# Kernel optimization log

Measured on AMD Instinct MI355X. Metric: run time of the kernel, lower is better.

Reference implementation:

```python
import jax, jax.numpy as jnp
import numpy as np

B_, L_, H_, N_ = 8, 1024, 1024, 64

def setup_inputs() -> dict:
    key = jax.random.key(0)
    k1, k2, k3, k4 = jax.random.split(key, 4)
    return {
        "samples": jax.random.normal(k1, (B_, L_, 3 * H_), dtype=jnp.float32),
        "label_one_hot": jax.random.uniform(k2, (B_, L_, N_), dtype=jnp.float32),
        "predict": jax.random.normal(k3, (B_, L_, N_), dtype=jnp.float32),
        "W": jax.random.normal(k4, (H_, 3 * H_), dtype=jnp.float32) * (1.0 / np.sqrt(3 * H_)),
        "b_proj": jnp.zeros((H_,), dtype=jnp.float32),
    }

def reference(samples, label_one_hot, predict, W, b_proj):
    # projection: Linear(3H -> H)
    s = jnp.einsum("blk,hk->blh", samples, W) + b_proj          # [b,L,H]
    # dense similarity graph with diagonal masked out, row-softmax
    graph = jnp.einsum("blh,bmh->blm", s, s)                     # [b,L,L]
    L = graph.shape[1]
    eye = jnp.eye(L, dtype=graph.dtype)
    A = jax.nn.softmax(graph - 1e5 * eye, axis=-1)               # [b,L,L]
    # centered masked labels
    sup = label_one_hot
    row_has = (jnp.sum(sup, axis=-1) > 0.5).astype(sup.dtype)    # [b,L]
    total = jnp.sum(row_has, axis=-1)[:, None]                   # [b,1]
    avg = (jnp.sum(sup, axis=-2) / total)[:, None, :]            # [b,1,N]
    B0 = (sup - avg) * row_has[..., None]                        # [b,L,N]
    # diagonal inverse-degree scaling (elementwise, no dense diag matmul)
    d = 1.0 / (jnp.sum(A, axis=-1) + 1e-10)                      # [b,L]
    P = d[:, :, None] * jnp.swapaxes(A, -1, -2)                  # [b,L,L]
    Db = d[:, :, None] * B0                                      # [b,L,N]
    # 6-step power-iteration scan with residual injection at t==3
    ut = jnp.zeros_like(B0)
    for t in range(1, 7):
        ut = jnp.einsum("blm,bmn->bln", P, ut) + Db
        if t == 3:
            ut = ut + predict  # dropout is identity in eval mode
    return ut

if __name__ == "__main__":
    out = reference(**setup_inputs())
    print(out.shape, out.dtype)
```

## Files before the change

### kernel.cpp

```cpp
#include <hip/hip_runtime.h>


typedef _Float16 f16_t;
typedef f16_t f16x4 __attribute__((ext_vector_type(4)));
typedef f16_t f16x8 __attribute__((ext_vector_type(8)));
typedef float floatx4 __attribute__((ext_vector_type(4)));

__device__ __forceinline__ void async_copy16(const void* g, void* l) {
  __builtin_amdgcn_global_load_lds(
      (const __attribute__((address_space(1))) void*)g,
      (__attribute__((address_space(3))) void*)l, 16, 0, 0);
}

__device__ __forceinline__ f16_t hi_of(float x) { return (f16_t)x; }
__device__ __forceinline__ f16_t lo_of(float x, f16_t h) {
  return (f16_t)(x - (float)h);
}

__global__ __launch_bounds__(256) void prep_kernel(
    const float* __restrict__ W, f16_t* __restrict__ Whi, f16_t* __restrict__ Wlo,
    const float* __restrict__ samples, f16_t* __restrict__ SampH)
{
  const int bx = blockIdx.x, tid = threadIdx.x;
  if (bx < 3072) {
    const int i = bx * 256 + tid;
    float4 v = ((const float4*)W)[i];
    v.x *= 32.f; v.y *= 32.f; v.z *= 32.f; v.w *= 32.f;
    f16x4 h, l;
    f16_t h0 = hi_of(v.x); h[0] = h0; l[0] = lo_of(v.x, h0);
    f16_t h1 = hi_of(v.y); h[1] = h1; l[1] = lo_of(v.y, h1);
    f16_t h2 = hi_of(v.z); h[2] = h2; l[2] = lo_of(v.z, h2);
    f16_t h3 = hi_of(v.w); h[3] = h3; l[3] = lo_of(v.w, h3);
    *(f16x4*)(Whi + (size_t)i * 4) = h;
    *(f16x4*)(Wlo + (size_t)i * 4) = l;
  } else {
    const int i = (bx - 3072) * 256 + tid;
    const float4 v = ((const float4*)samples)[i];
    f16x4 h;
    h[0] = (f16_t)v.x; h[1] = (f16_t)v.y; h[2] = (f16_t)v.z; h[3] = (f16_t)v.w;
    *(f16x4*)(SampH + (size_t)i * 4) = h;
  }
}

template <int CMODE>
__global__ __launch_bounds__(256) void gemm_mfma(
    const f16_t* __restrict__ AhiG,
    const f16_t* __restrict__ BhiG, const f16_t* __restrict__ BloG,
    const float* __restrict__ bias,
    float* __restrict__ Cf, f16_t* __restrict__ Chi, f16_t* __restrict__ Clo,
    int M, int N, int K, long long sA, long long sB, long long sC, float cscale)
{
  AhiG += (long long)blockIdx.z * sA;
  BhiG += (long long)blockIdx.z * sB;
  BloG += (long long)blockIdx.z * sB;
  if (CMODE == 1) Cf += (long long)blockIdx.z * sC;

  __shared__ __align__(16) char smem[49152];
  f16_t* AsHi = (f16_t*)smem;
  f16_t* BsHi = (f16_t*)(smem + 16384);
  f16_t* BsLo = (f16_t*)(smem + 32768);

  const int tid = threadIdx.x;
  const int lane = tid & 63;
  const int wave = tid >> 6;
  const int wm = wave >> 1, wn = wave & 1;

  int m0, n0;
  if (CMODE == 0) {
    m0 = blockIdx.y * 128;
    n0 = blockIdx.x * 128;
  } else {
    int idx = blockIdx.x, i = 0, accu = 0;
    while (accu + i + 1 <= idx) { accu += i + 1; ++i; }
    m0 = i * 128;
    n0 = (idx - accu) * 128;
  }

  const int fr = lane & 15;
  const int kg = (lane >> 4) * 8;
  const int aoff = (wm * 64 + fr) * 32 + kg;
  const int boff = (wn * 64 + fr) * 32 + kg;

  floatx4 acc[4][4] = {};

  for (int k0 = 0; k0 < K; k0 += 64) {
    __syncthreads();
#pragma unroll
    for (int it = 0; it < 4; ++it) {
      const int cb = it * 256 + wave * 64;
      const int c = cb + lane;
      const int kk = c >> 9;
      const int row = (c >> 2) & 127;
      const int kc = kk * 32 + (c & 3) * 8;
      const size_t ga = (size_t)(m0 + row) * K + k0 + kc;
      const size_t gb = (size_t)(n0 + row) * K + k0 + kc;
      async_copy16(AhiG + ga, (char*)AsHi + (size_t)cb * 16);
      async_copy16(BhiG + gb, (char*)BsHi + (size_t)cb * 16);
      async_copy16(BloG + gb, (char*)BsLo + (size_t)cb * 16);
    }
    __syncthreads();

#pragma unroll
    for (int kk = 0; kk < 2; ++kk) {
      f16x8 ah[4], bh[4], bl[4];
#pragma unroll
      for (int t = 0; t < 4; ++t) {
        ah[t] = *(const f16x8*)&AsHi[kk * 4096 + aoff + t * 512];
        bh[t] = *(const f16x8*)&BsHi[kk * 4096 + boff + t * 512];
        bl[t] = *(const f16x8*)&BsLo[kk * 4096 + boff + t * 512];
      }
#pragma unroll
      for (int i = 0; i < 4; ++i)
#pragma unroll
        for (int j = 0; j < 4; ++j) {
          acc[i][j] = __builtin_amdgcn_mfma_f32_16x16x32_f16(ah[i], bh[j], acc[i][j], 0, 0, 0);
          acc[i][j] = __builtin_amdgcn_mfma_f32_16x16x32_f16(ah[i], bl[j], acc[i][j], 0, 0, 0);
        }
    }
  }

  const int mr = (lane >> 4) * 4;
#pragma unroll
  for (int j = 0; j < 4; ++j) {
    const int n = n0 + wn * 64 + j * 16 + fr;
    const float bj = (CMODE == 0) ? bias[n] : 0.f;
#pragma unroll
    for (int i = 0; i < 4; ++i) {
#pragma unroll
      for (int r = 0; r < 4; ++r) {
        const int m = m0 + wm * 64 + i * 16 + mr + r;
        float v = acc[i][j][r];
        if (CMODE == 0) {
          v = v * cscale + bj;
          f16_t h = hi_of(v);
          Chi[(size_t)m * N + n] = h;
          Clo[(size_t)m * N + n] = lo_of(v, h);
        } else {
          if (m == n) v -= 1e5f;
          Cf[(size_t)m * N + n] = v;
        }
      }
    }
  }

  if (CMODE == 1 && m0 != n0) {
    float* T = (float*)smem;
#pragma unroll
    for (int mc = 0; mc < 4; ++mc) {
      __syncthreads();
      if (wm == (mc >> 1)) {
        const int ibase = (mc & 1) * 2;
#pragma unroll
        for (int di = 0; di < 2; ++di) {
#pragma unroll
          for (int j = 0; j < 4; ++j) {
            const int nl = wn * 64 + j * 16 + fr;
#pragma unroll
            for (int r = 0; r < 4; ++r) {
              const int mloc = di * 16 + mr + r;
              T[nl * 36 + mloc] = acc[ibase + di][j][r];
            }
          }
        }
      }
      __syncthreads();
      const int row = tid >> 1, half = tid & 1;
      const float* src = &T[row * 36 + half * 16];
      float* dst = Cf + (size_t)(n0 + row) * N + m0 + mc * 32 + half * 16;
#pragma unroll
      for (int q = 0; q < 16; ++q) dst[q] = src[q];
    }
  }
}

__global__ __launch_bounds__(256) void rowstats_kernel(
    const float* __restrict__ G, float* __restrict__ mx, float* __restrict__ inv)
{
  __shared__ float red[4];
  const int tid = threadIdx.x;
  const float* g = G + (size_t)blockIdx.x * 1024;
  const float4 v = ((const float4*)g)[tid];

  float m = fmaxf(fmaxf(v.x, v.y), fmaxf(v.z, v.w));
#pragma unroll
  for (int off = 32; off > 0; off >>= 1) m = fmaxf(m, __shfl_down(m, off));
  if ((tid & 63) == 0) red[tid >> 6] = m;
  __syncthreads();
  m = fmaxf(fmaxf(red[0], red[1]), fmaxf(red[2], red[3]));
  __syncthreads();

  float s = __expf(v.x - m) + __expf(v.y - m) + __expf(v.z - m) + __expf(v.w - m);
#pragma unroll
  for (int off = 32; off > 0; off >>= 1) s += __shfl_down(s, off);
  if ((tid & 63) == 0) red[tid >> 6] = s;
  __syncthreads();
  if (tid == 0) {
    mx[blockIdx.x] = m;
    inv[blockIdx.x] = 1.0f / (red[0] + red[1] + red[2] + red[3]);
  }
}

__global__ __launch_bounds__(256) void make_at_kernel(
    const float* __restrict__ G, const float* __restrict__ mx,
    const float* __restrict__ inv, f16_t* __restrict__ At)
{
  const int row = blockIdx.x;
  const int b = row >> 10;
  const int tid = threadIdx.x;
  const float4 g = ((const float4*)(G + (size_t)row * 1024))[tid];
  const float4 m = ((const float4*)(mx + b * 1024))[tid];
  const float4 iv = ((const float4*)(inv + b * 1024))[tid];
  f16x4 o;
  o[0] = (f16_t)(__expf(g.x - m.x) * iv.x);
  o[1] = (f16_t)(__expf(g.y - m.y) * iv.y);
  o[2] = (f16_t)(__expf(g.z - m.z) * iv.z);
  o[3] = (f16_t)(__expf(g.w - m.w) * iv.w);
  *(f16x4*)(At + (size_t)row * 1024 + tid * 4) = o;
}

__global__ __launch_bounds__(1024) void make_db_kernel(
    const float* __restrict__ sup, float* __restrict__ Db, f16_t* __restrict__ DbT)
{
  const int L = 1024, Nn = 64;
  const float* s = sup + (size_t)blockIdx.x * L * Nn;
  float* db = Db + (size_t)blockIdx.x * L * Nn;
  f16_t* dbt = DbT + (size_t)blockIdx.x * L * Nn;
  __shared__ float rowhas[1024];
  __shared__ float cpart[1024];
  __shared__ float tpart[16];
  __shared__ float avg[64];
  __shared__ float totalsh;
  const int tid = threadIdx.x;

  const float4* sr = (const float4*)(s + (size_t)tid * 64);
  float ss = 0.f;
#pragma unroll
  for (int i = 0; i < 16; ++i) { const float4 v = sr[i]; ss += (v.x + v.y) + (v.z + v.w); }
  const float rh = (ss > 0.5f) ? 1.f : 0.f;
  rowhas[tid] = rh;
  float t = rh;
#pragma unroll
  for (int off = 32; off > 0; off >>= 1) t += __shfl_down(t, off);
  if ((tid & 63) == 0) tpart[tid >> 6] = t;

  const int n = tid & 63, seg = tid >> 6;
  float cs = 0.f;
  for (int l = seg * 64; l < seg * 64 + 64; ++l) cs += s[(size_t)l * 64 + n];
  cpart[seg * 64 + n] = cs;
  __syncthreads();
  if (tid == 0) { float tt = 0.f; for (int i = 0; i < 16; ++i) tt += tpart[i]; totalsh = tt; }
  __syncthreads();
  if (tid < 64) {
    float a = 0.f;
    for (int i = 0; i < 16; ++i) a += cpart[i * 64 + tid];
    avg[tid] = a / totalsh;
  }
  __syncthreads();

  const float4* s4 = (const float4*)s;
  float4* d4 = (float4*)db;
  for (int i = tid; i < (L * Nn) / 4; i += 1024) {
    float4 v = s4[i];
    const int l = i >> 4;
    const int nb = (i & 15) * 4;
    const float rhl = rowhas[l];
    v.x = (v.x - avg[nb + 0]) * rhl;
    v.y = (v.y - avg[nb + 1]) * rhl;
    v.z = (v.z - avg[nb + 2]) * rhl;
    v.w = (v.w - avg[nb + 3]) * rhl;
    d4[i] = v;
  }
  for (int i = tid; i < L * Nn; i += 1024) {
    const int n2 = i >> 10, l2 = i & 1023;
    dbt[i] = (f16_t)((s[(size_t)l2 * 64 + n2] - avg[n2]) * rowhas[l2]);
  }
}

__global__ __launch_bounds__(256) void iter_part(
    const f16_t* __restrict__ At, const f16_t* __restrict__ UT,
    float* __restrict__ Part)
{
  const int L = 1024, Nn = 64;
  const int b = blockIdx.y, l0 = blockIdx.x * 64, ks = blockIdx.z;
  At += (size_t)b * L * L;
  UT += (size_t)b * Nn * L;
  Part += (((size_t)ks * 8 + b) * L) * Nn;

  __shared__ __align__(16) f16_t AtS[2 * 64 * 32];
  __shared__ __align__(16) f16_t UtS[2 * 64 * 32];

  const int tid = threadIdx.x;
  const int lane = tid & 63;
  const int wave = tid >> 6;
  const int fr = lane & 15;
  const int kg = (lane >> 4) * 8;

  floatx4 acc[4] = {};

  for (int mi = 0; mi < 4; ++mi) {
    const int m0 = ks * 256 + mi * 64;
    __syncthreads();
#pragma unroll
    for (int it = 0; it < 2; ++it) {
      const int cb = it * 256 + wave * 64;
      const int c = cb + lane;
      const int kk = c >> 8;
      const int row = (c >> 2) & 63;
      const int kc = kk * 32 + (c & 3) * 8;
      async_copy16(At + (size_t)(l0 + row) * L + m0 + kc, (char*)AtS + (size_t)cb * 16);
      async_copy16(UT + (size_t)row * L + m0 + kc, (char*)UtS + (size_t)cb * 16);
    }
    __syncthreads();
#pragma unroll
    for (int kk = 0; kk < 2; ++kk) {
      const f16x8 a = *(const f16x8*)&AtS[kk * 2048 + (wave * 16 + fr) * 32 + kg];
#pragma unroll
      for (int j = 0; j < 4; ++j) {
        const f16x8 bf = *(const f16x8*)&UtS[kk * 2048 + (j * 16 + fr) * 32 + kg];
        acc[j] = __builtin_amdgcn_mfma_f32_16x16x32_f16(a, bf, acc[j], 0, 0, 0);
      }
    }
  }

  const int mr = (lane >> 4) * 4;
#pragma unroll
  for (int j = 0; j < 4; ++j) {
    const int n = j * 16 + fr;
#pragma unroll
    for (int r = 0; r < 4; ++r) {
      const int l = wave * 16 + mr + r;
      Part[(size_t)(l0 + l) * Nn + n] = acc[j][r];
    }
  }
}

template <int PRED, int FINAL>
__global__ __launch_bounds__(256) void iter_fin(
    const float* __restrict__ Part, const float* __restrict__ Db,
    const float* __restrict__ Pred, f16_t* __restrict__ UTn,
    float* __restrict__ OutF)
{
  const int L = 1024, Nn = 64;
  const int b = blockIdx.y, l0 = blockIdx.x * 64;
  const size_t base = ((size_t)b * L + l0) * Nn;
  const size_t ksStride = (size_t)8 * L * Nn;
  Db += base;
  if (PRED) Pred += base;

  __shared__ f16_t OutS[64 * 72];
  const int tid = threadIdx.x;

#pragma unroll
  for (int it = 0; it < 4; ++it) {
    const int idx = it * 256 + tid;
    const int l = idx >> 4, n4 = (idx & 15) * 4;
    const size_t o = (size_t)l * Nn + n4;
    float4 v = *(const float4*)(Part + base + o);
    const float4 p1 = *(const float4*)(Part + base + ksStride + o);
    const float4 p2 = *(const float4*)(Part + base + 2 * ksStride + o);
    const float4 p3 = *(const float4*)(Part + base + 3 * ksStride + o);
    v.x += p1.x; v.y += p1.y; v.z += p1.z; v.w += p1.w;
    v.x += p2.x; v.y += p2.y; v.z += p2.z; v.w += p2.w;
    v.x += p3.x; v.y += p3.y; v.z += p3.z; v.w += p3.w;
    const float4 d = *(const float4*)(Db + o);
    v.x += d.x; v.y += d.y; v.z += d.z; v.w += d.w;
    if (PRED) {
      const float4 p = *(const float4*)(Pred + o);
      v.x += p.x; v.y += p.y; v.z += p.z; v.w += p.w;
    }
    if (FINAL) {
      *(float4*)(OutF + base + o) = v;
    } else {
      OutS[(n4 + 0) * 72 + l] = (f16_t)v.x;
      OutS[(n4 + 1) * 72 + l] = (f16_t)v.y;
      OutS[(n4 + 2) * 72 + l] = (f16_t)v.z;
      OutS[(n4 + 3) * 72 + l] = (f16_t)v.w;
    }
  }
  if (!FINAL) {
    __syncthreads();
    f16_t* dst = UTn + (size_t)b * Nn * L;
#pragma unroll
    for (int it = 0; it < 2; ++it) {
      const int c = it * 256 + tid;
      const int n = c >> 3, lc = (c & 7) * 8;
      *(f16x8*)(dst + (size_t)n * L + l0 + lc) = *(const f16x8*)&OutS[n * 72 + lc];
    }
  }
}

extern "C" void kernel_launch(void* const* d_in, const int* in_sizes, int n_in,
                              void* d_out, int out_size, void* d_ws, size_t ws_size,
                              hipStream_t stream) {
  const float* samples = (const float*)d_in[0];
  const float* label   = (const float*)d_in[1];
  const float* predict = (const float*)d_in[2];
  const float* W       = (const float*)d_in[3];
  const float* bproj   = (const float*)d_in[4];
  float* out = (float*)d_out;

  char* ws = (char*)d_ws;
  f16_t* Whi = (f16_t*)ws;
  f16_t* Wlo = (f16_t*)(ws + 6291456);
  float* mx  = (float*)ws;
  float* inv = (float*)(ws + 32768);
  float* Db  = (float*)(ws + 65536);
  f16_t* DbT = (f16_t*)(ws + 65536 + 2097152);
  f16_t* UTa = (f16_t*)(ws + 65536 + 3145728);
  f16_t* UTb = (f16_t*)(ws + 65536 + 4194304);
  f16_t* SampH = (f16_t*)(ws + 12582912);
  float* G     = (float*)(ws + 12582912);
  f16_t* Shi = (f16_t*)(ws + 62914560);
  f16_t* Slo = (f16_t*)(ws + 62914560 + 16777216);
  f16_t* At  = Shi;
  float* Part = (float*)Slo;

  const long long LH = 1024LL * 1024;
  const long long LL = 1024LL * 1024;

  prep_kernel<<<dim3(27648), 256, 0, stream>>>(W, Whi, Wlo, samples, SampH);

  gemm_mfma<0><<<dim3(8, 64, 1), 256, 0, stream>>>(
      SampH, Whi, Wlo, bproj, nullptr, Shi, Slo,
      8192, 1024, 3072, 0, 0, 0, 1.0f / 32.0f);

  gemm_mfma<1><<<dim3(36, 1, 8), 256, 0, stream>>>(
      Shi, Shi, Slo, nullptr, G, nullptr, nullptr,
      1024, 1024, 1024, LH, LH, LL, 1.0f);

  rowstats_kernel<<<8192, 256, 0, stream>>>(G, mx, inv);
  make_at_kernel<<<8192, 256, 0, stream>>>(G, mx, inv, At);

  make_db_kernel<<<8, 1024, 0, stream>>>(label, Db, DbT);

  dim3 gp(16, 8, 4), gf(16, 8);
  iter_part<<<gp, 256, 0, stream>>>(At, DbT, Part);
  iter_fin<0, 0><<<gf, 256, 0, stream>>>(Part, Db, nullptr, UTa, nullptr);
  iter_part<<<gp, 256, 0, stream>>>(At, UTa, Part);
  iter_fin<1, 0><<<gf, 256, 0, stream>>>(Part, Db, predict, UTb, nullptr);
  iter_part<<<gp, 256, 0, stream>>>(At, UTb, Part);
  iter_fin<0, 0><<<gf, 256, 0, stream>>>(Part, Db, nullptr, UTa, nullptr);
  iter_part<<<gp, 256, 0, stream>>>(At, UTa, Part);
  iter_fin<0, 0><<<gf, 256, 0, stream>>>(Part, Db, nullptr, UTb, nullptr);
  iter_part<<<gp, 256, 0, stream>>>(At, UTb, Part);
  iter_fin<0, 1><<<gf, 256, 0, stream>>>(Part, Db, nullptr, nullptr, out);
}
```

Measured before the change: 422.1 us.

## Add dedicated 256x128 multi-stage async-LDS GEMM for input projection

Replaces the generic templated MFMA GEMM used for the samples-by-W projection with a specialized kernel. It uses 512 threads, a 256x128 output tile and a 4-slot LDS ring that keeps three stages of global-to-LDS async copies in flight. It also uses swizzled LDS addressing and raises wave priority around the MFMA bursts. The aim is to hide global-load latency and improve data reuse per block, at the cost of 128KB of LDS per block (one block per CU) and a grid of only 256 blocks. The wrap-around prefetch on the last stages issues loads that are never used.

```diff
diff --git a/kernel.cpp b/kernel.cpp
--- a/kernel.cpp
+++ b/kernel.cpp
@@ -42,6 +42,125 @@
   }
 }
 
+__global__ __launch_bounds__(512, 2) void gemm1_8ph(
+    const f16_t* __restrict__ Ag,
+    const f16_t* __restrict__ BhG, const f16_t* __restrict__ BlG,
+    const float* __restrict__ bias,
+    f16_t* __restrict__ Chi, f16_t* __restrict__ Clo,
+    int N, int K, float cscale)
+{
+  __shared__ __align__(16) char smem[131072];
+
+  const int tid = threadIdx.x;
+  const int lane = tid & 63;
+  const int wave = tid >> 6;
+  const int wm = wave >> 2;
+  const int wn = wave & 3;
+  const int m0 = blockIdx.y * 256;
+  const int n0 = blockIdx.x * 128;
+  const int fr = lane & 15;
+  const int lch = lane >> 4;
+
+  const int gA0 = tid;
+  const int gA1 = tid + 512;
+  const int rA0 = gA0 >> 2, lcA0 = (gA0 & 3) ^ (rA0 & 3);
+  const int rA1 = gA1 >> 2, lcA1 = (gA1 & 3) ^ (rA1 & 3);
+  const int rB = tid >> 2, lcB = (tid & 3) ^ (rB & 3);
+  const f16_t* aSrc0 = Ag + (size_t)(m0 + rA0) * K + lcA0 * 8;
+  const f16_t* aSrc1 = Ag + (size_t)(m0 + rA1) * K + lcA1 * 8;
+  const f16_t* bhSrc = BhG + (size_t)(n0 + rB) * K + lcB * 8;
+  const f16_t* blSrc = BlG + (size_t)(n0 + rB) * K + lcB * 8;
+  char* ldsA0 = smem + gA0 * 16;
+  char* ldsA1 = smem + gA1 * 16;
+  char* ldsBh = smem + 16384 + (size_t)tid * 16;
+  char* ldsBl = smem + 24576 + (size_t)tid * 16;
+
+  const int swz = ((lch ^ (fr & 3)) * 16);
+  const int aoff = (wm * 128 + fr) * 64 + swz;
+  const int boff = (wn * 32 + fr) * 64 + swz;
+
+  floatx4 acc[8][2] = {};
+
+#pragma unroll
+  for (int s = 0; s < 3; ++s) {
+    const int slot = s * 32768;
+    const int k0 = s * 32;
+    async_copy16(aSrc0 + k0, ldsA0 + slot);
+    async_copy16(aSrc1 + k0, ldsA1 + slot);
+    async_copy16(bhSrc + k0, ldsBh + slot);
+    async_copy16(blSrc + k0, ldsBl + slot);
+  }
+
+  const int NS = K >> 5;
+  for (int s = 0; s < NS; ++s) {
+    asm volatile("s_waitcnt vmcnt(8)" ::: "memory");
+    __builtin_amdgcn_s_barrier();
+
+    const char* base = smem + (s & 3) * 32768;
+
+    f16x8 bh0 = *(const f16x8*)(base + 16384 + boff);
+    f16x8 bh1 = *(const f16x8*)(base + 16384 + boff + 1024);
+    f16x8 bl0 = *(const f16x8*)(base + 24576 + boff);
+    f16x8 bl1 = *(const f16x8*)(base + 24576 + boff + 1024);
+    f16x8 a0[4];
+#pragma unroll
+    for (int i = 0; i < 4; ++i) a0[i] = *(const f16x8*)(base + aoff + i * 1024);
+
+    {
+      int ss = s + 3; if (ss >= NS) ss -= NS;
+      const int slot = (ss & 3) * 32768;
+      const int k0 = ss * 32;
+      async_copy16(aSrc0 + k0, ldsA0 + slot);
+      async_copy16(aSrc1 + k0, ldsA1 + slot);
+      async_copy16(bhSrc + k0, ldsBh + slot);
+      async_copy16(blSrc + k0, ldsBl + slot);
+    }
+
+    __builtin_amdgcn_s_setprio(1);
+#pragma unroll
+    for (int i = 0; i < 4; ++i) {
+      acc[i][0] = __builtin_amdgcn_mfma_f32_16x16x32_f16(a0[i], bh0, acc[i][0], 0, 0, 0);
+      acc[i][1] = __builtin_amdgcn_mfma_f32_16x16x32_f16(a0[i], bh1, acc[i][1], 0, 0, 0);
+      acc[i][0] = __builtin_amdgcn_mfma_f32_16x16x32_f16(a0[i], bl0, acc[i][0], 0, 0, 0);
+      acc[i][1] = __builtin_amdgcn_mfma_f32_16x16x32_f16(a0[i], bl1, acc[i][1], 0, 0, 0);
+    }
+    __builtin_amdgcn_s_setprio(0);
+
+    f16x8 a1[4];
+#pragma unroll
+    for (int i = 0; i < 4; ++i) a1[i] = *(const f16x8*)(base + aoff + 4096 + i * 1024);
+
+    __builtin_amdgcn_s_setprio(1);
+#pragma unroll
+    for (int i = 0; i < 4; ++i) {
+      acc[i + 4][0] = __builtin_amdgcn_mfma_f32_16x16x32_f16(a1[i], bh0, acc[i + 4][0], 0, 0, 0);
+      acc[i + 4][1] = __builtin_amdgcn_mfma_f32_16x16x32_f16(a1[i], bh1, acc[i + 4][1], 0, 0, 0);
+      acc[i + 4][0] = __builtin_amdgcn_mfma_f32_16x16x32_f16(a1[i], bl0, acc[i + 4][0], 0, 0, 0);
+      acc[i + 4][1] = __builtin_amdgcn_mfma_f32_16x16x32_f16(a1[i], bl1, acc[i + 4][1], 0, 0, 0);
+    }
+    __builtin_amdgcn_s_setprio(0);
+  }
+  asm volatile("s_waitcnt vmcnt(0)" ::: "memory");
+
+  const int mr = (lane >> 4) * 4;
+#pragma unroll
+  for (int j = 0; j < 2; ++j) {
+    const int n = n0 + wn * 32 + j * 16 + fr;
+    const float bj = bias[n];
+#pragma unroll
+    for (int i = 0; i < 8; ++i) {
+#pragma unroll
+      for (int r = 0; r < 4; ++r) {
+        const int m = m0 + wm * 128 + i * 16 + mr + r;
+        float v = acc[i][j][r] * cscale + bj;
+        f16_t h = hi_of(v);
+        Chi[(size_t)m * N + n] = h;
+        Clo[(size_t)m * N + n] = lo_of(v, h);
+      }
+    }
+  }
+}
+
 template <int CMODE>
 __global__ __launch_bounds__(256) void gemm_mfma(
     const f16_t* __restrict__ AhiG,
@@ -420,9 +539,8 @@
 
   prep_kernel<<<dim3(27648), 256, 0, stream>>>(W, Whi, Wlo, samples, SampH);
 
-  gemm_mfma<0><<<dim3(8, 64, 1), 256, 0, stream>>>(
-      SampH, Whi, Wlo, bproj, nullptr, Shi, Slo,
-      8192, 1024, 3072, 0, 0, 0, 1.0f / 32.0f);
+  gemm1_8ph<<<dim3(8, 32), 512, 0, stream>>>(
+      SampH, Whi, Wlo, bproj, Shi, Slo, 1024, 3072, 1.0f / 32.0f);
 
   gemm_mfma<1><<<dim3(36, 1, 8), 256, 0, stream>>>(
       Shi, Shi, Slo, nullptr, G, nullptr, nullptr,
```

Result: faster. 407.8 us (-3.4%).
